# Kernel optimization log

Measured on AMD Instinct MI355X. Metric: run time of the kernel, lower is better.

Reference implementation:

```python
import jax, jax.numpy as jnp
import numpy as np

B, D, K, L, C = 1024, 512, 255, 256, 80  # batch, feat, internal nodes, leaves, classes
DEPTH = 8  # complete binary tree: 2^8 = 256 leaves


def _build_res_path():
    # res_path[l, k] = 1 if internal node k is on leaf l's path and leaf goes left,
    # -1 if it goes right, 0 if node k not on the path (matches build_tree_squeeze).
    rp = np.zeros((L, K), dtype=np.int32)
    for leaf in range(L):
        node = 0
        for d in range(DEPTH):
            bit = (leaf >> (DEPTH - 1 - d)) & 1  # 0 -> left, 1 -> right
            rp[leaf, node] = 1 if bit == 0 else -1
            node = 2 * node + 1 + bit
    return jnp.asarray(rp)


def setup_inputs() -> dict:
    key = jax.random.key(0)
    k1, k2, k3, k4 = jax.random.split(key, 4)
    x = jax.random.normal(k1, (B, D), dtype=jnp.float32)
    node_embeddings = jax.random.normal(k2, (K, D), dtype=jnp.float32)
    leaf_W = jax.random.normal(k3, (L * C, D), dtype=jnp.float32) * (1.0 / np.sqrt(D))
    leaf_b = jax.random.normal(k4, (L * C,), dtype=jnp.float32) * 0.01
    res_path = _build_res_path()
    return {"x": x, "node_embeddings": node_embeddings, "leaf_W": leaf_W,
            "leaf_b": leaf_b, "res_path": res_path}


def reference(x, node_embeddings, leaf_W, leaf_b, res_path):
    # L2-normalize node embeddings, cosine-sim routing probabilities
    ne = node_embeddings / jnp.linalg.norm(node_embeddings, axis=-1, keepdims=True)
    node_sim = jax.nn.sigmoid(jnp.einsum('bc,kc->bk', x, ne))  # [B, K]
    # leaf decision logits: Linear(D, L*C) reshaped to [B, L, C]
    leaf_dec = (jnp.einsum('bc,oc->bo', x, leaf_W) + leaf_b).reshape(x.shape[0], L, C)
    left_mask = (res_path == 1)[None]    # [1, L, K]
    right_mask = (res_path == -1)[None]  # [1, L, K]
    ns = node_sim[:, None, :]            # [B, 1, K]
    prob_left = jnp.prod(jnp.where(left_mask, ns, 1.0), axis=-1)        # [B, L]
    prob_right = jnp.prod(jnp.where(right_mask, 1.0 - ns, 1.0), axis=-1)  # [B, L]
    probs = (prob_left * prob_right)[..., None] * leaf_dec  # [B, L, C]
    return probs.sum(axis=1), node_sim
```

## Files before the change

kernel.cpp:

```cpp
#include <hip/hip_runtime.h>
#include <stdint.h>

#define B_  1024
#define D_  512
#define K_  255
#define L_  256
#define C_  80

typedef __attribute__((ext_vector_type(8))) short bf16x8;
typedef __attribute__((ext_vector_type(4))) float f32x4;
typedef __attribute__((ext_vector_type(8))) short short8;

#define GLD(gsrc, ldst) \
  __builtin_amdgcn_global_load_lds((const __attribute__((address_space(1))) void*)(gsrc), \
                                   (__attribute__((address_space(3))) void*)(ldst), 16, 0, 0)

__device__ __forceinline__ short cvt_bf16(float f) {
    unsigned u = __float_as_uint(f);
    u += 0x7FFFu + ((u >> 16) & 1u);
    return (short)(u >> 16);
}

__global__ __launch_bounds__(256) void convert_kernel(const float* __restrict__ w,
                                                      const float* __restrict__ x,
                                                      const float* __restrict__ ne,
                                                      short* __restrict__ wb,
                                                      short* __restrict__ xb,
                                                      short* __restrict__ neb) {
    __shared__ float red[256];
    const int tid = threadIdx.x;
    if (blockIdx.x < 2048) {
        size_t i0 = (size_t)blockIdx.x * 256 + tid;
        const size_t stride = 2048u * 256u;
        for (size_t v = i0; v < 1310720u; v += stride) {
            float4 a = ((const float4*)w)[v * 2];
            float4 b = ((const float4*)w)[v * 2 + 1];
            short8 o;
            o[0] = cvt_bf16(a.x); o[1] = cvt_bf16(a.y); o[2] = cvt_bf16(a.z); o[3] = cvt_bf16(a.w);
            o[4] = cvt_bf16(b.x); o[5] = cvt_bf16(b.y); o[6] = cvt_bf16(b.z); o[7] = cvt_bf16(b.w);
            ((short8*)wb)[v] = o;
        }
        for (size_t v = i0; v < 65536u; v += stride) {
            float4 a = ((const float4*)x)[v * 2];
            float4 b = ((const float4*)x)[v * 2 + 1];
            short8 o;
            o[0] = cvt_bf16(a.x); o[1] = cvt_bf16(a.y); o[2] = cvt_bf16(a.z); o[3] = cvt_bf16(a.w);
            o[4] = cvt_bf16(b.x); o[5] = cvt_bf16(b.y); o[6] = cvt_bf16(b.z); o[7] = cvt_bf16(b.w);
            ((short8*)xb)[v] = o;
        }
    } else {
        const int row = blockIdx.x - 2048;
        if (row == 255) {
            ((unsigned*)(neb + 255 * 512))[tid] = 0u;
            return;
        }
        const float2* nr = (const float2*)(ne + (size_t)row * 512);
        float2 a = nr[tid];
        red[tid] = a.x * a.x + a.y * a.y;
        __syncthreads();
        #pragma unroll
        for (int s = 128; s > 0; s >>= 1) {
            if (tid < s) red[tid] += red[tid + s];
            __syncthreads();
        }
        float inv = rsqrtf(red[0]);
        unsigned lo = (unsigned short)cvt_bf16(a.x * inv);
        unsigned hi = (unsigned short)cvt_bf16(a.y * inv);
        ((unsigned*)(neb + (size_t)row * 512))[tid] = lo | (hi << 16);
    }
}

__global__ __launch_bounds__(256) void simgemm_kernel(const short* __restrict__ xb,
                                                      const short* __restrict__ neb,
                                                      float* __restrict__ out1) {
    __shared__ __align__(16) short Ald[512 * 8];
    __shared__ __align__(16) short Bld[512 * 8];
    const int tid = threadIdx.x;
    const int lane = tid & 63, wave = tid >> 6;
    const int q = lane >> 4, r = lane & 15;
    const int mt = blockIdx.x >> 2;
    const int nt = blockIdx.x & 3;

    f32x4 acc[4];
    #pragma unroll
    for (int nf = 0; nf < 4; ++nf) acc[nf] = (f32x4){0.f, 0.f, 0.f, 0.f};

    const bf16x8* Av = (const bf16x8*)Ald;
    const bf16x8* Bv = (const bf16x8*)Bld;

    for (int kb = 0; kb < 8; ++kb) {
        __syncthreads();
        #pragma unroll
        for (int j = 0; j < 2; ++j) {
            int ph = j * 256 + tid, rr = ph >> 3, g = (ph & 7) ^ (rr & 7);
            GLD(xb + ((size_t)(mt * 64 + rr) * D_ + kb * 64 + g * 8), Ald + ph * 8);
        }
        #pragma unroll
        for (int j = 0; j < 2; ++j) {
            int ph = j * 256 + tid, cc = ph >> 3, g = (ph & 7) ^ (cc & 7);
            GLD(neb + ((size_t)(nt * 64 + cc) * D_ + kb * 64 + g * 8), Bld + ph * 8);
        }
        __syncthreads();
        #pragma unroll
        for (int ks = 0; ks < 2; ++ks) {
            const int g = ks * 4 + q;
            int rl = wave * 16 + r;
            bf16x8 af = Av[rl * 8 + (g ^ (rl & 7))];
            #pragma unroll
            for (int nf = 0; nf < 4; ++nf) {
                int cl = nf * 16 + r;
                bf16x8 bfr = Bv[cl * 8 + (g ^ (cl & 7))];
                acc[nf] = __builtin_amdgcn_mfma_f32_16x16x32_bf16(af, bfr, acc[nf], 0, 0, 0);
            }
        }
    }
    #pragma unroll
    for (int nf = 0; nf < 4; ++nf) {
        int gcol = nt * 64 + nf * 16 + r;
        if (gcol < K_) {
            #pragma unroll
            for (int i = 0; i < 4; ++i) {
                int grow = mt * 64 + wave * 16 + q * 4 + i;
                out1[(size_t)grow * K_ + gcol] = 1.f / (1.f + __expf(-acc[nf][i]));
            }
        }
    }
}

__global__ __launch_bounds__(256) void leafprob_kernel(const float* __restrict__ out1,
                                                       float* __restrict__ p_ws,
                                                       float* __restrict__ out0) {
    __shared__ float ss[K_];
    const int b = blockIdx.x, t = threadIdx.x;
    if (t < K_) ss[t] = out1[(size_t)b * K_ + t];
    if (t < C_) out0[(size_t)b * C_ + t] = 0.f;
    __syncthreads();
    float prob = 1.f;
    int node = 0;
    #pragma unroll
    for (int d = 0; d < 8; ++d) {
        int bit = (t >> (7 - d)) & 1;
        float s = ss[node];
        prob *= bit ? (1.f - s) : s;
        node = 2 * node + 1 + bit;
    }
    p_ws[(size_t)b * L_ + t] = prob;
}

__global__ __launch_bounds__(256, 2) void gemm_kernel(const short* __restrict__ xb,
                                                      const short* __restrict__ wb,
                                                      const float* __restrict__ p,
                                                      const float* __restrict__ lb,
                                                      float* __restrict__ partial) {
    __shared__ __align__(16) short Ald[1024 * 8];
    __shared__ __align__(16) short Bld[640 * 8];
    __shared__ __align__(16) float p_t[4][128];

    const int tid = threadIdx.x;
    const int lane = tid & 63, wave = tid >> 6;
    const int q = lane >> 4, r = lane & 15;
    const int wrow = wave * 32;
    const int lc = blockIdx.x & 63;
    const int mt = blockIdx.x >> 6;

    if (tid < 128) {
        float4 pw = *(const float4*)(p + (size_t)(mt * 128 + tid) * L_ + lc * 4);
        p_t[0][tid] = pw.x; p_t[1][tid] = pw.y;
        p_t[2][tid] = pw.z; p_t[3][tid] = pw.w;
    }
    __syncthreads();

    f32x4 outacc[2][5];
    #pragma unroll
    for (int mf = 0; mf < 2; ++mf) {
        const int base = wrow + mf * 16 + q * 4;
        f32x4 pf[4];
        #pragma unroll
        for (int li = 0; li < 4; ++li) pf[li] = *(const f32x4*)&p_t[li][base];
        #pragma unroll
        for (int nf = 0; nf < 5; ++nf) {
            f32x4 s = pf[0] * lb[(size_t)(lc * 4 + 0) * C_ + nf * 16 + r];
            s += pf[1] * lb[(size_t)(lc * 4 + 1) * C_ + nf * 16 + r];
            s += pf[2] * lb[(size_t)(lc * 4 + 2) * C_ + nf * 16 + r];
            s += pf[3] * lb[(size_t)(lc * 4 + 3) * C_ + nf * 16 + r];
            outacc[mf][nf] = s;
        }
    }

    const bf16x8* Av = (const bf16x8*)Ald;
    const bf16x8* Bv = (const bf16x8*)Bld;
    const f32x4 z4 = {0.f, 0.f, 0.f, 0.f};

    for (int kb = 0; kb < 8; ++kb) {
        for (int li = 0; li < 4; ++li) {
            __syncthreads();
            if (li == 0) {
                #pragma unroll
                for (int j = 0; j < 4; ++j) {
                    int ph = j * 256 + tid;
                    int rr = ph >> 3;
                    int g  = (ph & 7) ^ (rr & 7);
                    GLD(xb + ((size_t)(mt * 128 + rr) * D_ + kb * 64 + g * 8), Ald + ph * 8);
                }
            }
            #pragma unroll
            for (int j = 0; j < 2; ++j) {
                int ph = j * 256 + tid;
                int cc = ph >> 3;
                int g  = (ph & 7) ^ (cc & 7);
                GLD(wb + ((size_t)((lc * 4 + li) * C_ + cc) * D_ + kb * 64 + g * 8), Bld + ph * 8);
            }
            if (tid < 128) {
                int ph = 512 + tid;
                int cc = ph >> 3;
                int g  = (ph & 7) ^ (cc & 7);
                GLD(wb + ((size_t)((lc * 4 + li) * C_ + cc) * D_ + kb * 64 + g * 8), Bld + ph * 8);
            }
            __syncthreads();

            f32x4 dec[2][5];
            #pragma unroll
            for (int ks = 0; ks < 2; ++ks) {
                const int g = ks * 4 + q;
                bf16x8 af[2], bfr[5];
                #pragma unroll
                for (int mf = 0; mf < 2; ++mf) {
                    int rl = wrow + mf * 16 + r;
                    af[mf] = Av[rl * 8 + (g ^ (rl & 7))];
                }
                #pragma unroll
                for (int nf = 0; nf < 5; ++nf) {
                    int cl = nf * 16 + r;
                    bfr[nf] = Bv[cl * 8 + (g ^ (cl & 7))];
                }
                #pragma unroll
                for (int mf = 0; mf < 2; ++mf)
                    #pragma unroll
                    for (int nf = 0; nf < 5; ++nf)
                        dec[mf][nf] = __builtin_amdgcn_mfma_f32_16x16x32_bf16(
                            af[mf], bfr[nf], ks == 0 ? z4 : dec[mf][nf], 0, 0, 0);
            }

            #pragma unroll
            for (int mf = 0; mf < 2; ++mf) {
                f32x4 pf4 = *(const f32x4*)&p_t[li][wrow + mf * 16 + q * 4];
                #pragma unroll
                for (int nf = 0; nf < 5; ++nf)
                    outacc[mf][nf] += pf4 * dec[mf][nf];
            }
        }
    }

    const size_t rbase = (size_t)lc * B_ + mt * 128;
    #pragma unroll
    for (int mf = 0; mf < 2; ++mf)
        #pragma unroll
        for (int nf = 0; nf < 5; ++nf)
            #pragma unroll
            for (int i = 0; i < 4; ++i) {
                int row = wrow + mf * 16 + q * 4 + i;
                int col = nf * 16 + r;
                partial[(rbase + row) * C_ + col] = outacc[mf][nf][i];
            }
}

__global__ __launch_bounds__(256) void reduce_kernel(const float* __restrict__ partial,
                                                     float* __restrict__ out0) {
    const int chunk = blockIdx.x >> 3;
    const int jg    = blockIdx.x & 7;
    const int idx   = chunk * 256 + threadIdx.x;
    const float4* p4 = (const float4*)partial;
    float4 s = {0.f, 0.f, 0.f, 0.f};
    #pragma unroll
    for (int j = 0; j < 8; ++j) {
        float4 v = p4[(size_t)(jg * 8 + j) * (B_ * C_ / 4) + idx];
        s.x += v.x; s.y += v.y; s.z += v.z; s.w += v.w;
    }
    float* o = out0 + (size_t)idx * 4;
    atomicAdd(o + 0, s.x);
    atomicAdd(o + 1, s.y);
    atomicAdd(o + 2, s.z);
    atomicAdd(o + 3, s.w);
}

extern "C" void kernel_launch(void* const* d_in, const int* in_sizes, int n_in,
                              void* d_out, int out_size, void* d_ws, size_t ws_size,
                              hipStream_t stream) {
    const float* x  = (const float*)d_in[0];
    const float* ne = (const float*)d_in[1];
    const float* lW = (const float*)d_in[2];
    const float* lb = (const float*)d_in[3];

    float* out0 = (float*)d_out;
    float* out1 = out0 + (size_t)B_ * C_;

    char* ws = (char*)d_ws;
    short* xb      = (short*)ws;
    short* neb     = (short*)(ws + (1u << 20));
    float* p_ws    = (float*)(ws + (1u << 20) + (1u << 18));
    short* wb      = (short*)(ws + (9u << 18));
    float* partial = (float*)(ws + (24u << 20));

    convert_kernel<<<2304, 256, 0, stream>>>(lW, x, ne, wb, xb, neb);
    simgemm_kernel<<<64, 256, 0, stream>>>(xb, neb, out1);
    leafprob_kernel<<<B_, 256, 0, stream>>>(out1, p_ws, out0);
    gemm_kernel<<<512, 256, 0, stream>>>(xb, wb, p_ws, lb, partial);
    reduce_kernel<<<640, 256, 0, stream>>>(partial, out0);
}
```

Measured before the change: 142.7 us.

## Fuse leaf_W bf16 conversion into GEMM with register-staged prefetch

Drops the separate pass that converts the 42MB leaf_W matrix to bf16 in workspace. The GEMM kernel now loads fp32 W tiles into registers, converts them to bf16 and writes them to LDS, prefetching the next tile while MFMAs run. The K tile is doubled to 128 with a 16-way swizzle, halving the k-loop trip count. Each W element is still read once per M tile (8 times in total), now as fp32 instead of bf16, so GEMM-side traffic doubles; LDS use and register pressure also grow.

New measurement: 143.1 us. About the same (+0.3%).

```diff
diff --git a/kernel.cpp b/kernel.cpp
--- a/kernel.cpp
+++ b/kernel.cpp
@@ -21,35 +21,26 @@
     return (short)(u >> 16);
 }
 
-__global__ __launch_bounds__(256) void convert_kernel(const float* __restrict__ w,
-                                                      const float* __restrict__ x,
+__device__ __forceinline__ short8 cvt8(float4 a, float4 b) {
+    short8 o;
+    o[0] = cvt_bf16(a.x); o[1] = cvt_bf16(a.y); o[2] = cvt_bf16(a.z); o[3] = cvt_bf16(a.w);
+    o[4] = cvt_bf16(b.x); o[5] = cvt_bf16(b.y); o[6] = cvt_bf16(b.z); o[7] = cvt_bf16(b.w);
+    return o;
+}
+
+__global__ __launch_bounds__(256) void convert_kernel(const float* __restrict__ x,
                                                       const float* __restrict__ ne,
-                                                      short* __restrict__ wb,
                                                       short* __restrict__ xb,
                                                       short* __restrict__ neb) {
     __shared__ float red[256];
     const int tid = threadIdx.x;
-    if (blockIdx.x < 2048) {
-        size_t i0 = (size_t)blockIdx.x * 256 + tid;
-        const size_t stride = 2048u * 256u;
-        for (size_t v = i0; v < 1310720u; v += stride) {
-            float4 a = ((const float4*)w)[v * 2];
-            float4 b = ((const float4*)w)[v * 2 + 1];
-            short8 o;
-            o[0] = cvt_bf16(a.x); o[1] = cvt_bf16(a.y); o[2] = cvt_bf16(a.z); o[3] = cvt_bf16(a.w);
-            o[4] = cvt_bf16(b.x); o[5] = cvt_bf16(b.y); o[6] = cvt_bf16(b.z); o[7] = cvt_bf16(b.w);
-            ((short8*)wb)[v] = o;
-        }
-        for (size_t v = i0; v < 65536u; v += stride) {
-            float4 a = ((const float4*)x)[v * 2];
-            float4 b = ((const float4*)x)[v * 2 + 1];
-            short8 o;
-            o[0] = cvt_bf16(a.x); o[1] = cvt_bf16(a.y); o[2] = cvt_bf16(a.z); o[3] = cvt_bf16(a.w);
-            o[4] = cvt_bf16(b.x); o[5] = cvt_bf16(b.y); o[6] = cvt_bf16(b.z); o[7] = cvt_bf16(b.w);
-            ((short8*)xb)[v] = o;
-        }
+    if (blockIdx.x < 256) {
+        size_t v = (size_t)blockIdx.x * 256 + tid;
+        float4 a = ((const float4*)x)[v * 2];
+        float4 b = ((const float4*)x)[v * 2 + 1];
+        ((short8*)xb)[v] = cvt8(a, b);
     } else {
-        const int row = blockIdx.x - 2048;
+        const int row = blockIdx.x - 256;
         if (row == 255) {
             ((unsigned*)(neb + 255 * 512))[tid] = 0u;
             return;
@@ -148,12 +139,12 @@
 }
 
 __global__ __launch_bounds__(256, 2) void gemm_kernel(const short* __restrict__ xb,
-                                                      const short* __restrict__ wb,
+                                                      const float* __restrict__ lW,
                                                       const float* __restrict__ p,
                                                       const float* __restrict__ lb,
                                                       float* __restrict__ partial) {
-    __shared__ __align__(16) short Ald[1024 * 8];
-    __shared__ __align__(16) short Bld[640 * 8];
+    __shared__ __align__(16) short Ald[2048 * 8];
+    __shared__ __align__(16) short Bld[1280 * 8];
     __shared__ __align__(16) float p_t[4][128];
 
     const int tid = threadIdx.x;
@@ -163,6 +154,28 @@
     const int lc = blockIdx.x & 63;
     const int mt = blockIdx.x >> 6;
 
+    float4 bq[10];
+    auto loadB = [&](int l, int kb) {
+        #pragma unroll
+        for (int j = 0; j < 5; ++j) {
+            int ph = j * 256 + tid;
+            int cc = ph >> 4;
+            int g  = (ph & 15) ^ (cc & 15);
+            const float4* s = (const float4*)(lW + ((size_t)(l * C_ + cc)) * D_ + kb * 128 + g * 8);
+            bq[2 * j]     = s[0];
+            bq[2 * j + 1] = s[1];
+        }
+    };
+    auto writeB = [&]() {
+        #pragma unroll
+        for (int j = 0; j < 5; ++j) {
+            int ph = j * 256 + tid;
+            ((short8*)Bld)[ph] = cvt8(bq[2 * j], bq[2 * j + 1]);
+        }
+    };
+
+    loadB(lc * 4 + 0, 0);
+
     if (tid < 128) {
         float4 pw = *(const float4*)(p + (size_t)(mt * 128 + tid) * L_ + lc * 4);
         p_t[0][tid] = pw.x; p_t[1][tid] = pw.y;
@@ -191,47 +204,41 @@
     const bf16x8* Bv = (const bf16x8*)Bld;
     const f32x4 z4 = {0.f, 0.f, 0.f, 0.f};
 
-    for (int kb = 0; kb < 8; ++kb) {
+    for (int kb = 0; kb < 4; ++kb) {
         for (int li = 0; li < 4; ++li) {
             __syncthreads();
+            writeB();
             if (li == 0) {
                 #pragma unroll
-                for (int j = 0; j < 4; ++j) {
+                for (int j = 0; j < 8; ++j) {
                     int ph = j * 256 + tid;
-                    int rr = ph >> 3;
-                    int g  = (ph & 7) ^ (rr & 7);
-                    GLD(xb + ((size_t)(mt * 128 + rr) * D_ + kb * 64 + g * 8), Ald + ph * 8);
+                    int rr = ph >> 4;
+                    int g  = (ph & 15) ^ (rr & 15);
+                    GLD(xb + ((size_t)(mt * 128 + rr) * D_ + kb * 128 + g * 8), Ald + ph * 8);
                 }
             }
-            #pragma unroll
-            for (int j = 0; j < 2; ++j) {
-                int ph = j * 256 + tid;
-                int cc = ph >> 3;
-                int g  = (ph & 7) ^ (cc & 7);
-                GLD(wb + ((size_t)((lc * 4 + li) * C_ + cc) * D_ + kb * 64 + g * 8), Bld + ph * 8);
-            }
-            if (tid < 128) {
-                int ph = 512 + tid;
-                int cc = ph >> 3;
-                int g  = (ph & 7) ^ (cc & 7);
-                GLD(wb + ((size_t)((lc * 4 + li) * C_ + cc) * D_ + kb * 64 + g * 8), Bld + ph * 8);
-            }
             __syncthreads();
 
+            {
+                int nkb = kb, nli = li + 1;
+                if (nli == 4) { nli = 0; ++nkb; }
+                if (nkb < 4) loadB(lc * 4 + nli, nkb);
+            }
+
             f32x4 dec[2][5];
             #pragma unroll
-            for (int ks = 0; ks < 2; ++ks) {
+            for (int ks = 0; ks < 4; ++ks) {
                 const int g = ks * 4 + q;
                 bf16x8 af[2], bfr[5];
                 #pragma unroll
                 for (int mf = 0; mf < 2; ++mf) {
                     int rl = wrow + mf * 16 + r;
-                    af[mf] = Av[rl * 8 + (g ^ (rl & 7))];
+                    af[mf] = Av[rl * 16 + (g ^ (rl & 15))];
                 }
                 #pragma unroll
                 for (int nf = 0; nf < 5; ++nf) {
                     int cl = nf * 16 + r;
-                    bfr[nf] = Bv[cl * 8 + (g ^ (cl & 7))];
+                    bfr[nf] = Bv[cl * 16 + (g ^ (cl & 15))];
                 }
                 #pragma unroll
                 for (int mf = 0; mf < 2; ++mf)
@@ -298,12 +305,11 @@
     short* xb      = (short*)ws;
     short* neb     = (short*)(ws + (1u << 20));
     float* p_ws    = (float*)(ws + (1u << 20) + (1u << 18));
-    short* wb      = (short*)(ws + (9u << 18));
     float* partial = (float*)(ws + (24u << 20));
 
-    convert_kernel<<<2304, 256, 0, stream>>>(lW, x, ne, wb, xb, neb);
+    convert_kernel<<<512, 256, 0, stream>>>(x, ne, xb, neb);
     simgemm_kernel<<<64, 256, 0, stream>>>(xb, neb, out1);
     leafprob_kernel<<<B_, 256, 0, stream>>>(out1, p_ws, out0);
-    gemm_kernel<<<512, 256, 0, stream>>>(xb, wb, p_ws, lb, partial);
+    gemm_kernel<<<512, 256, 0, stream>>>(xb, lW, p_ws, lb, partial);
     reduce_kernel<<<640, 256, 0, stream>>>(partial, out0);
 }
```
